# Performance work log

Measured on AMD Instinct MI355X. Metric: run time of the kernel, lower is better.

Reference implementation:

```python
import jax, jax.numpy as jnp
import numpy as np

TAU_PRE = 2.0
TAU_POST = 2.0


def setup_inputs() -> dict:
    key = jax.random.key(0)
    k1, k2, k3 = jax.random.split(key, 3)
    T, B, PRE, POST = 64, 16, 4096, 4096
    in_spikes = jax.random.uniform(k1, (T, B, PRE), dtype=jnp.float32)
    out_spikes = jax.random.uniform(k2, (T, B, POST), dtype=jnp.float32)
    weight = jax.random.normal(k3, (POST, PRE), dtype=jnp.float32)
    return {"in_spikes": in_spikes, "out_spikes": out_spikes, "weight": weight}


def reference(in_spikes, out_spikes, weight):
    # in_spikes: [T, B, pre]; out_spikes: [T, B, post]; weight: [post, pre]
    T, B, PRE = in_spikes.shape
    POST = out_spikes.shape[-1]

    def step(carry, xs):
        trace_pre, trace_post, delta_w = carry
        i_sp, o_sp = xs
        trace_pre = jnp.clip(trace_pre - trace_pre / TAU_PRE + i_sp, 0.0, 1.0)  # [B, pre]
        trace_post = trace_post - trace_post / TAU_POST + o_sp  # [B, post]
        # sum_b o[b,post]*trace_pre[b,pre] - (sum_b o[b,post]*trace_post[b,post]) * w[post,pre]
        dw = (jnp.einsum('bo,bp->op', o_sp, trace_pre)
              - (o_sp * trace_post).sum(0)[:, None] * weight)
        return (trace_pre, trace_post, delta_w + dw), None

    init = (jnp.zeros((B, PRE), in_spikes.dtype),
            jnp.zeros((B, POST), out_spikes.dtype),
            jnp.zeros((POST, PRE), weight.dtype))
    (trace_pre, trace_post, delta_w), _ = jax.lax.scan(step, init, (in_spikes, out_spikes))
    return delta_w
```

## Files before the change

### kernel.cpp

```cpp
#include <hip/hip_runtime.h>


#define T_STEPS 64
#define B_SZ    16
#define PRE     4096
#define POST    4096
#define K_TOT   1024

typedef __attribute__((ext_vector_type(8))) unsigned short ushort8;
typedef __attribute__((ext_vector_type(8))) __bf16 bf16x8;
typedef __attribute__((ext_vector_type(4))) float floatx4;

__device__ __forceinline__ unsigned short f2bf(float f) {
    unsigned int u = __float_as_uint(f);
    u += 0x7fff + ((u >> 16) & 1);
    return (unsigned short)(u >> 16);
}

__device__ __forceinline__ void glds16(const void* g, void* l) {
    __builtin_amdgcn_global_load_lds((const __attribute__((address_space(1))) void*)g,
                                     (__attribute__((address_space(3))) void*)l,
                                     16, 0, 0);
}

__global__ __launch_bounds__(256) void trace_convert(
        const float* __restrict__ in_spikes,
        const float* __restrict__ out_spikes,
        unsigned short* __restrict__ AT,
        unsigned short* __restrict__ BT,
        float* __restrict__ coef) {
    __shared__ float ldsf[4096];
    __shared__ unsigned short ot[128 * 34];
    __shared__ float cbuf[8][33];
    const int tid  = threadIdx.x;
    const int wave = tid >> 6;
    const int lane = tid & 63;
    const bool isA = blockIdx.x >= 128;
    const int p0 = (blockIdx.x & 127) * 32;
    const float* src = isA ? out_spikes : in_spikes;
    unsigned short* dst = isA ? AT : BT;

    const int bA = tid >> 5;
    const int pA = tid & 31;

    float st0 = 0.f, st1 = 0.f, c0 = 0.f, c1 = 0.f;

    for (int tc = 0; tc < 8; ++tc) {
        const int T0 = tc * 8;
        #pragma unroll
        for (int i = 0; i < 4; ++i) {
            const int q  = (wave * 4 + i) * 64 + lane;
            const int p  = (q & 7) * 4;
            const int b  = (q >> 3) & 15;
            const int tl = q >> 7;
            const float* g = src + ((size_t)((T0 + tl) * 16 + b)) * 4096 + p0 + p;
            glds16(g, (char*)ldsf + (size_t)(wave * 4 + i) * 1024);
        }
        __syncthreads();

        #pragma unroll
        for (int tl = 0; tl < 8; ++tl) {
            const float x0 = ldsf[tl * 512 + bA * 32 + pA];
            const float x1 = ldsf[tl * 512 + (bA + 8) * 32 + pA];
            if (isA) {
                st0 = 0.5f * st0 + x0; c0 += x0 * st0;
                st1 = 0.5f * st1 + x1; c1 += x1 * st1;
                ot[(tl * 16 + bA)     * 34 + pA] = f2bf(x0);
                ot[(tl * 16 + bA + 8) * 34 + pA] = f2bf(x1);
            } else {
                st0 = fminf(fmaxf(0.5f * st0 + x0, 0.f), 1.f);
                st1 = fminf(fmaxf(0.5f * st1 + x1, 0.f), 1.f);
                ot[(tl * 16 + bA)     * 34 + pA] = f2bf(st0);
                ot[(tl * 16 + bA + 8) * 34 + pA] = f2bf(st1);
            }
        }
        __syncthreads();

        const int pf = tid >> 3;
        const int c8 = tid & 7;
        #pragma unroll
        for (int i = 0; i < 2; ++i) {
            const int ch = c8 + i * 8;
            ushort8 v;
            #pragma unroll
            for (int s = 0; s < 8; ++s) v[s] = ot[(ch * 8 + s) * 34 + pf];
            *(ushort8*)&dst[(size_t)(p0 + pf) * K_TOT + T0 * 16 + ch * 8] = v;
        }
    }

    if (isA) {
        cbuf[bA][pA] = c0 + c1;
        __syncthreads();
        if (tid < 32) {
            float s = 0.f;
            #pragma unroll
            for (int r = 0; r < 8; ++r) s += cbuf[r][tid];
            coef[p0 + tid] = s;
        }
    }
}

#define BK 64

__global__ __launch_bounds__(256) void stdp_gemm_mfma(
        const unsigned short* __restrict__ AT,
        const unsigned short* __restrict__ BT,
        const float* __restrict__ W,
        const float* __restrict__ coef,
        float* __restrict__ Cout) {
    __shared__ unsigned short As[128][BK];
    __shared__ unsigned short Bs[128][BK];
    const int tid  = threadIdx.x;
    const int lane = tid & 63;
    const int wave = tid >> 6;
    const int wm = (wave >> 1) * 64;
    const int wn = (wave & 1) * 64;
    const int m0 = blockIdx.y * 128;
    const int n0 = blockIdx.x * 128;

    floatx4 acc[4][4];
    #pragma unroll
    for (int i = 0; i < 4; ++i)
        #pragma unroll
        for (int j = 0; j < 4; ++j)
            acc[i][j] = (floatx4){0.f, 0.f, 0.f, 0.f};

    const int srow = tid >> 3;
    const int qg   = (tid & 7) ^ (srow & 7);
    const unsigned short* ga = &AT[(size_t)(m0 + srow) * K_TOT + qg * 8];
    const unsigned short* gb = &BT[(size_t)(n0 + srow) * K_TOT + qg * 8];
    char* laB = (char*)&As[0][0] + wave * 1024;
    char* lbB = (char*)&Bs[0][0] + wave * 1024;

    const int rm = lane & 15;
    const int q  = lane >> 4;
    const int sw = rm & 7;

    for (int k0 = 0; k0 < K_TOT; k0 += BK) {
        #pragma unroll
        for (int i = 0; i < 4; ++i) {
            glds16(ga + (size_t)i * 32 * K_TOT, laB + i * 4096);
            glds16(gb + (size_t)i * 32 * K_TOT, lbB + i * 4096);
        }
        ga += BK; gb += BK;
        __syncthreads();

        #pragma unroll
        for (int h = 0; h < 2; ++h) {
            const int ks = ((h * 4 + q) ^ sw) * 8;
            bf16x8 af[4], bv[4];
            #pragma unroll
            for (int i = 0; i < 4; ++i) {
                af[i] = *(const bf16x8*)&As[wm + i * 16 + rm][ks];
                bv[i] = *(const bf16x8*)&Bs[wn + i * 16 + rm][ks];
            }
            #pragma unroll
            for (int mi = 0; mi < 4; ++mi)
                #pragma unroll
                for (int ni = 0; ni < 4; ++ni)
                    acc[mi][ni] = __builtin_amdgcn_mfma_f32_16x16x32_bf16(
                        af[mi], bv[ni], acc[mi][ni], 0, 0, 0);
        }
        __syncthreads();
    }

    const int colp = n0 + wn + rm;
    const int rowb = m0 + wm + (lane >> 4) * 4;
    #pragma unroll
    for (int mi = 0; mi < 4; ++mi) {
        #pragma unroll
        for (int r = 0; r < 4; ++r) {
            const int o = rowb + mi * 16 + r;
            const float cf = coef[o];
            const float* wr = &W[(size_t)o * PRE];
            float* cr = &Cout[(size_t)o * PRE];
            #pragma unroll
            for (int ni = 0; ni < 4; ++ni) {
                const int p = colp + ni * 16;
                cr[p] = acc[mi][ni][r] - cf * wr[p];
            }
        }
    }
}

extern "C" void kernel_launch(void* const* d_in, const int* in_sizes, int n_in,
                              void* d_out, int out_size, void* d_ws, size_t ws_size,
                              hipStream_t stream) {
    const float* in_spikes  = (const float*)d_in[0];
    const float* out_spikes = (const float*)d_in[1];
    const float* weight     = (const float*)d_in[2];
    float* out = (float*)d_out;

    unsigned short* AT = (unsigned short*)d_ws;
    unsigned short* BT = AT + (size_t)POST * K_TOT;
    float* coef = (float*)(BT + (size_t)PRE * K_TOT);

    trace_convert<<<256, 256, 0, stream>>>(in_spikes, out_spikes, AT, BT, coef);

    dim3 grid(PRE / 128, POST / 128);
    stdp_gemm_mfma<<<grid, 256, 0, stream>>>(AT, BT, weight, coef, out);
}
```

Before: 184.3 us.

## Double-buffer GEMM LDS, remap blocks, and rework trace conversion kernel

The GEMM now double-buffers its LDS tiles so the global-to-LDS loads for the next K step overlap the current MFMA work. It also remaps the 1D grid so that consecutive blocks land on different XCDs, raises MFMA issue priority, and uses nontemporal loads and stores for the weight read and output write. The trace conversion kernel is rewritten to use 512 blocks of 16 columns, register-prefetched direct global loads and a smaller padded LDS transpose. In exchange the GEMM uses twice the LDS per block, and the nontemporal hints and remap depend on cache behaviour.

```diff
diff --git a/kernel.cpp b/kernel.cpp
--- a/kernel.cpp
+++ b/kernel.cpp
@@ -29,72 +29,71 @@
         unsigned short* __restrict__ AT,
         unsigned short* __restrict__ BT,
         float* __restrict__ coef) {
-    __shared__ float ldsf[4096];
-    __shared__ unsigned short ot[128 * 34];
-    __shared__ float cbuf[8][33];
+    __shared__ unsigned short ot[128 * 17];
+    __shared__ float cbuf[16 * 17];
     const int tid  = threadIdx.x;
-    const int wave = tid >> 6;
-    const int lane = tid & 63;
-    const bool isA = blockIdx.x >= 128;
-    const int p0 = (blockIdx.x & 127) * 32;
+    const bool isA = blockIdx.x >= 256;
+    const int p0 = (blockIdx.x & 255) * 16;
     const float* src = isA ? out_spikes : in_spikes;
     unsigned short* dst = isA ? AT : BT;
 
-    const int bA = tid >> 5;
-    const int pA = tid & 31;
-
-    float st0 = 0.f, st1 = 0.f, c0 = 0.f, c1 = 0.f;
-
-    for (int tc = 0; tc < 8; ++tc) {
-        const int T0 = tc * 8;
-        #pragma unroll
-        for (int i = 0; i < 4; ++i) {
-            const int q  = (wave * 4 + i) * 64 + lane;
-            const int p  = (q & 7) * 4;
-            const int b  = (q >> 3) & 15;
-            const int tl = q >> 7;
-            const float* g = src + ((size_t)((T0 + tl) * 16 + b)) * 4096 + p0 + p;
-            glds16(g, (char*)ldsf + (size_t)(wave * 4 + i) * 1024);
-        }
-        __syncthreads();
-
+    const int p = tid & 15;
+    const int b = tid >> 4;
+    const float* gbase = src + (size_t)b * PRE + p0 + p;
+
+    const int pf = tid >> 4;
+    const int ch = tid & 15;
+    unsigned short* dstf = &dst[(size_t)(p0 + pf) * K_TOT + ch * 8];
+
+    float x[2][8];
+    float st = 0.f, c0 = 0.f;
+
+    #pragma unroll
+    for (int tl = 0; tl < 8; ++tl) x[0][tl] = gbase[(size_t)tl * 65536];
+
+    #pragma unroll
+    for (int c = 0; c < 8; ++c) {
+        if (c < 7) {
+            #pragma unroll
+            for (int tl = 0; tl < 8; ++tl)
+                x[(c + 1) & 1][tl] = gbase[(size_t)((c + 1) * 8 + tl) * 65536];
+        }
         #pragma unroll
         for (int tl = 0; tl < 8; ++tl) {
-            const float x0 = ldsf[tl * 512 + bA * 32 + pA];
-            const float x1 = ldsf[tl * 512 + (bA + 8) * 32 + pA];
+            const float xv = x[c & 1][tl];
+            unsigned short ov;
             if (isA) {
-                st0 = 0.5f * st0 + x0; c0 += x0 * st0;
-                st1 = 0.5f * st1 + x1; c1 += x1 * st1;
-                ot[(tl * 16 + bA)     * 34 + pA] = f2bf(x0);
-                ot[(tl * 16 + bA + 8) * 34 + pA] = f2bf(x1);
+                st = 0.5f * st + xv;
+                c0 += xv * st;
+                ov = f2bf(xv);
             } else {
-                st0 = fminf(fmaxf(0.5f * st0 + x0, 0.f), 1.f);
-                st1 = fminf(fmaxf(0.5f * st1 + x1, 0.f), 1.f);
-                ot[(tl * 16 + bA)     * 34 + pA] = f2bf(st0);
-                ot[(tl * 16 + bA + 8) * 34 + pA] = f2bf(st1);
+                st = fminf(fmaxf(0.5f * st + xv, 0.f), 1.f);
+                ov = f2bf(st);
             }
-        }
-        __syncthreads();
-
-        const int pf = tid >> 3;
-        const int c8 = tid & 7;
-        #pragma unroll
-        for (int i = 0; i < 2; ++i) {
-            const int ch = c8 + i * 8;
-            ushort8 v;
-            #pragma unroll
-            for (int s = 0; s < 8; ++s) v[s] = ot[(ch * 8 + s) * 34 + pf];
-            *(ushort8*)&dst[(size_t)(p0 + pf) * K_TOT + T0 * 16 + ch * 8] = v;
-        }
+            ot[(tl * 16 + b) * 17 + p] = ov;
+        }
+        asm volatile("s_waitcnt lgkmcnt(0)" ::: "memory");
+        __builtin_amdgcn_s_barrier();
+        __builtin_amdgcn_sched_barrier(0);
+
+        ushort8 v;
+        #pragma unroll
+        for (int s = 0; s < 8; ++s) v[s] = ot[(ch * 8 + s) * 17 + pf];
+        *(ushort8*)&dstf[c * 128] = v;
+
+        asm volatile("s_waitcnt lgkmcnt(0)" ::: "memory");
+        __builtin_amdgcn_s_barrier();
+        __builtin_amdgcn_sched_barrier(0);
     }
 
     if (isA) {
-        cbuf[bA][pA] = c0 + c1;
-        __syncthreads();
-        if (tid < 32) {
+        cbuf[b * 17 + p] = c0;
+        asm volatile("s_waitcnt lgkmcnt(0)" ::: "memory");
+        __builtin_amdgcn_s_barrier();
+        if (tid < 16) {
             float s = 0.f;
             #pragma unroll
-            for (int r = 0; r < 8; ++r) s += cbuf[r][tid];
+            for (int r = 0; r < 16; ++r) s += cbuf[r * 17 + tid];
             coef[p0 + tid] = s;
         }
     }
@@ -102,21 +101,24 @@
 
 #define BK 64
 
-__global__ __launch_bounds__(256) void stdp_gemm_mfma(
+__global__ __launch_bounds__(256, 2) void stdp_gemm_mfma(
         const unsigned short* __restrict__ AT,
         const unsigned short* __restrict__ BT,
         const float* __restrict__ W,
         const float* __restrict__ coef,
         float* __restrict__ Cout) {
-    __shared__ unsigned short As[128][BK];
-    __shared__ unsigned short Bs[128][BK];
+    __shared__ unsigned short As[2][128][BK];
+    __shared__ unsigned short Bs[2][128][BK];
     const int tid  = threadIdx.x;
     const int lane = tid & 63;
     const int wave = tid >> 6;
     const int wm = (wave >> 1) * 64;
     const int wn = (wave & 1) * 64;
-    const int m0 = blockIdx.y * 128;
-    const int n0 = blockIdx.x * 128;
+
+    const int bid = blockIdx.x;
+    const int f   = (bid & 7) * 128 + (bid >> 3);
+    const int m0  = (f >> 5) * 128;
+    const int n0  = (f & 31) * 128;
 
     floatx4 acc[4][4];
     #pragma unroll
@@ -129,40 +131,52 @@
     const int qg   = (tid & 7) ^ (srow & 7);
     const unsigned short* ga = &AT[(size_t)(m0 + srow) * K_TOT + qg * 8];
     const unsigned short* gb = &BT[(size_t)(n0 + srow) * K_TOT + qg * 8];
-    char* laB = (char*)&As[0][0] + wave * 1024;
-    char* lbB = (char*)&Bs[0][0] + wave * 1024;
 
     const int rm = lane & 15;
     const int q  = lane >> 4;
     const int sw = rm & 7;
 
-    for (int k0 = 0; k0 < K_TOT; k0 += BK) {
-        #pragma unroll
-        for (int i = 0; i < 4; ++i) {
-            glds16(ga + (size_t)i * 32 * K_TOT, laB + i * 4096);
-            glds16(gb + (size_t)i * 32 * K_TOT, lbB + i * 4096);
-        }
-        ga += BK; gb += BK;
-        __syncthreads();
-
+    #define STAGE(t, buf)                                                      \
+        do {                                                                   \
+            char* laB_ = (char*)&As[buf][0][0] + wave * 1024;                  \
+            char* lbB_ = (char*)&Bs[buf][0][0] + wave * 1024;                  \
+            const unsigned short* ga_ = ga + (t) * BK;                         \
+            const unsigned short* gb_ = gb + (t) * BK;                         \
+            _Pragma("unroll")                                                  \
+            for (int i_ = 0; i_ < 4; ++i_) {                                   \
+                glds16(ga_ + (size_t)i_ * 32 * K_TOT, laB_ + i_ * 4096);       \
+                glds16(gb_ + (size_t)i_ * 32 * K_TOT, lbB_ + i_ * 4096);       \
+            }                                                                  \
+        } while (0)
+
+    STAGE(0, 0);
+    __syncthreads();
+
+    #pragma unroll
+    for (int t = 0; t < K_TOT / BK; ++t) {
+        const int buf = t & 1;
+        if (t + 1 < K_TOT / BK) STAGE(t + 1, buf ^ 1);
         #pragma unroll
         for (int h = 0; h < 2; ++h) {
             const int ks = ((h * 4 + q) ^ sw) * 8;
             bf16x8 af[4], bv[4];
             #pragma unroll
             for (int i = 0; i < 4; ++i) {
-                af[i] = *(const bf16x8*)&As[wm + i * 16 + rm][ks];
-                bv[i] = *(const bf16x8*)&Bs[wn + i * 16 + rm][ks];
+                af[i] = *(const bf16x8*)&As[buf][wm + i * 16 + rm][ks];
+                bv[i] = *(const bf16x8*)&Bs[buf][wn + i * 16 + rm][ks];
             }
+            __builtin_amdgcn_s_setprio(1);
             #pragma unroll
             for (int mi = 0; mi < 4; ++mi)
                 #pragma unroll
                 for (int ni = 0; ni < 4; ++ni)
                     acc[mi][ni] = __builtin_amdgcn_mfma_f32_16x16x32_bf16(
                         af[mi], bv[ni], acc[mi][ni], 0, 0, 0);
+            __builtin_amdgcn_s_setprio(0);
         }
         __syncthreads();
     }
+    #undef STAGE
 
     const int colp = n0 + wn + rm;
     const int rowb = m0 + wm + (lane >> 4) * 4;
@@ -177,7 +191,8 @@
             #pragma unroll
             for (int ni = 0; ni < 4; ++ni) {
                 const int p = colp + ni * 16;
-                cr[p] = acc[mi][ni][r] - cf * wr[p];
+                const float wv = __builtin_nontemporal_load(&wr[p]);
+                __builtin_nontemporal_store(acc[mi][ni][r] - cf * wv, &cr[p]);
             }
         }
     }
@@ -195,8 +210,7 @@
     unsigned short* BT = AT + (size_t)POST * K_TOT;
     float* coef = (float*)(BT + (size_t)PRE * K_TOT);
 
-    trace_convert<<<256, 256, 0, stream>>>(in_spikes, out_spikes, AT, BT, coef);
-
-    dim3 grid(PRE / 128, POST / 128);
-    stdp_gemm_mfma<<<grid, 256, 0, stream>>>(AT, BT, weight, coef, out);
-}
+    trace_convert<<<512, 256, 0, stream>>>(in_spikes, out_spikes, AT, BT, coef);
+
+    stdp_gemm_mfma<<<1024, 256, 0, stream>>>(AT, BT, weight, coef, out);
+}
```

New measurement: 186.4 us. No clear change (+1.1%).
